# Optimization experiments

Measured on AMD Instinct MI355X. Metric: run time of the kernel, lower is better.

The kernel has to match this reference:

```python
import jax, jax.numpy as jnp
import numpy as np

B, LQ, LK, DK, DV = 32, 128, 4096, 256, 256


def setup_inputs() -> dict:
    key = jax.random.key(0)
    k1, k2, k3, k4, k5 = jax.random.split(key, 5)
    return {
        "query": jax.random.normal(k1, (B, LQ, DK), dtype=jnp.float32),
        "query_lengths": jax.random.randint(k2, (B,), 1, LQ, dtype=jnp.int32),
        "keys": jax.random.normal(k3, (B, LK, DK), dtype=jnp.float32),
        "values": jax.random.normal(k4, (B, LK, DV), dtype=jnp.float32),
        "mask": jax.random.randint(k5, (B, LK), 0, 2, dtype=jnp.int32),  # 1 = masked out
    }


def reference(query, query_lengths, keys, values, mask):
    # zero query positions beyond each example's length (torch: mask_query masked_fill 0)
    q_valid = jnp.arange(query.shape[1])[None, :] < query_lengths[:, None]  # [B, Lq]
    query = jnp.where(q_valid[:, :, None], query, 0.0)
    # zero masked key/value timesteps (torch mask: 1 -> masked)
    kv_valid = (mask == 0)[:, :, None]  # [B, Lk, 1]
    keys = jnp.where(kv_valid, keys, 0.0)
    values = jnp.where(kv_valid, values, 0.0)
    # attention scores [B, Lq, Lk]
    weights = jnp.einsum("bqd,bkd->bqk", query, keys)
    # exact-zero scores (masked rows/cols) -> -inf, matching torch weights==0.0 fill
    weights = jnp.where(weights == 0.0, -jnp.inf, weights)
    weights = jax.nn.softmax(weights, axis=-1)
    # rows that were all -inf produce NaN -> cleaned to 0
    weights = jnp.where(jnp.isnan(weights), 0.0, weights)
    attended = jnp.einsum("bqk,bkv->bqv", weights, values)  # [B, Lq, Dv]
    return jnp.mean(attended, axis=1)  # [B, Dv]
```

## Files before the change

kernel.cpp:

```cpp
#include <hip/hip_runtime.h>
#include <hip/hip_fp16.h>
#include <stdint.h>

#define NB  32
#define NLQ 128
#define NLK 4096
#define NDK 256
#define NDV 256
#define KT  32
#define SPLITS 8
#define MINSPLITS 4

typedef _Float16 f16;
typedef _Float16 f16x4 __attribute__((ext_vector_type(4)));
typedef _Float16 f16x8 __attribute__((ext_vector_type(8)));
typedef float    f32x4 __attribute__((ext_vector_type(4)));

__global__ __launch_bounds__(512) void fvta_part1(
    const float* __restrict__ q_, const float* __restrict__ k_,
    const float* __restrict__ v_, const int* __restrict__ mask_,
    f16* __restrict__ accw, float* __restrict__ mlw)
{
    __shared__ __align__(16) f16 KA[2][KT * NDK];
    __shared__ __align__(16) f16 QA[64 * NDK];
    __shared__ int MK[NLK / MINSPLITS];

    const int tid = threadIdx.x, w = tid >> 6, lane = tid & 63;
    const int l15 = lane & 15, lhi = lane >> 4;
    const int qsub = w >> 1;
    const int dvh  = w & 1;
    const int x = blockIdx.x, b = blockIdx.y;
    const int S = gridDim.x >> 1;
    const int s = x >> 1, qz = x & 1;
    const int slice = NLK / S, nt = slice / KT, kbase = s * slice;
    const float NEG = -__builtin_inff();

    const float* kb = k_ + ((size_t)b * NLK + kbase) * NDK;
    const float* vb = v_ + ((size_t)b * NLK + kbase) * NDV;
    const int*   mb = mask_ + b * NLK + kbase;

    for (int i = tid; i < slice; i += 512) MK[i] = mb[i];

    {
        const float* qsrc = q_ + ((size_t)b * NLQ + qz * 64) * NDK;
        #pragma unroll
        for (int r = 0; r < 8; ++r) {
            const int idx = r * 512 + tid;
            const int qq  = idx >> 6;
            const int d   = (idx & 63) * 4;
            f32x4 xv = *(const f32x4*)(qsrc + qq * NDK + d);
            f16x4 hh; hh[0]=(f16)xv[0]; hh[1]=(f16)xv[1]; hh[2]=(f16)xv[2]; hh[3]=(f16)xv[3];
            *(f16x4*)(QA + qq * NDK + (d ^ ((qq & 15) << 3))) = hh;
        }
    }

    f32x4 accu[8];
    #pragma unroll
    for (int i = 0; i < 8; ++i) accu[i] = (f32x4){0.f, 0.f, 0.f, 0.f};
    float m_run = NEG, l_run = 0.f;

    f32x4 ks[4];

    auto stage = [&](f16* KAb) {
        #pragma unroll
        for (int r = 0; r < 4; ++r) {
            const int idx = r * 512 + tid;
            const int kk  = idx >> 6;
            const int d   = (idx & 63) * 4;
            const int e   = kk * NDK + (d ^ ((kk & 15) << 3));
            f32x4 xv = ks[r];
            f16x4 hh; hh[0]=(f16)xv[0]; hh[1]=(f16)xv[1]; hh[2]=(f16)xv[2]; hh[3]=(f16)xv[3];
            *(f16x4*)(KAb + e) = hh;
        }
    };

    #pragma unroll
    for (int r = 0; r < 4; ++r)
        ks[r] = *(const f32x4*)(kb + (r * 512 + tid) * 4);
    stage(KA[0]);
    __syncthreads();

    const int swz = l15 << 3;

    for (int t = 0; t < nt; ++t) {
        const int cur = t & 1;
        if (t + 1 < nt) {
            const float* ksrc = kb + (size_t)(t + 1) * KT * NDK;
            #pragma unroll
            for (int r = 0; r < 4; ++r)
                ks[r] = *(const f32x4*)(ksrc + (r * 512 + tid) * 4);
        }
        const int k0 = t * KT;

        f32x4 s4a = (f32x4){0.f,0.f,0.f,0.f}, s4b = s4a;
        {
            const f16* k0p = &KA[cur][(0 * 16 + l15) * NDK];
            const f16* k1p = &KA[cur][(1 * 16 + l15) * NDK];
            const f16* qp  = &QA[(qsub * 16 + l15) * NDK];
            #pragma unroll
            for (int kd = 0; kd < 8; ++kd) {
                const int col = (kd * 32 + lhi * 8) ^ swz;
                f16x8 qv  = *(const f16x8*)(qp + col);
                f16x8 kfa = *(const f16x8*)(k0p + col);
                s4a = __builtin_amdgcn_mfma_f32_16x16x32_f16(kfa, qv, s4a, 0, 0, 0);
                f16x8 kfb = *(const f16x8*)(k1p + col);
                s4b = __builtin_amdgcn_mfma_f32_16x16x32_f16(kfb, qv, s4b, 0, 0, 0);
            }
        }

        const int4 m4a = *(const int4*)(MK + k0 + lhi * 4);
        const int4 m4b = *(const int4*)(MK + k0 + 16 + lhi * 4);
        float sa[4], sb[4];
        sa[0] = m4a.x ? NEG : s4a[0]; sa[1] = m4a.y ? NEG : s4a[1];
        sa[2] = m4a.z ? NEG : s4a[2]; sa[3] = m4a.w ? NEG : s4a[3];
        sb[0] = m4b.x ? NEG : s4b[0]; sb[1] = m4b.y ? NEG : s4b[1];
        sb[2] = m4b.z ? NEG : s4b[2]; sb[3] = m4b.w ? NEG : s4b[3];

        float tmax = fmaxf(fmaxf(fmaxf(sa[0], sa[1]), fmaxf(sa[2], sa[3])),
                           fmaxf(fmaxf(sb[0], sb[1]), fmaxf(sb[2], sb[3])));
        tmax = fmaxf(tmax, __shfl_xor(tmax, 16, 64));
        tmax = fmaxf(tmax, __shfl_xor(tmax, 32, 64));

        const bool defer = (m_run != NEG) && __all(tmax - m_run <= 8.f);
        if (!defer) {
            const float mnew = fmaxf(m_run, tmax);
            if (mnew != NEG) {
                const float scale = (m_run == NEG) ? 0.f : __expf(m_run - mnew);
                float scj[4];
                #pragma unroll
                for (int j = 0; j < 4; ++j) scj[j] = __shfl(scale, lhi * 4 + j, 64);
                #pragma unroll
                for (int d = 0; d < 8; ++d) {
                    accu[d][0] *= scj[0]; accu[d][1] *= scj[1];
                    accu[d][2] *= scj[2]; accu[d][3] *= scj[3];
                }
                l_run *= scale;
                m_run = mnew;
            }
        }

        float p4a[4], p4b[4];
        if (m_run == NEG) {
            #pragma unroll
            for (int j = 0; j < 4; ++j) { p4a[j] = 0.f; p4b[j] = 0.f; }
        } else {
            #pragma unroll
            for (int j = 0; j < 4; ++j) {
                p4a[j] = __expf(sa[j] - m_run);
                p4b[j] = __expf(sb[j] - m_run);
            }
        }
        float ps = (p4a[0] + p4a[1]) + (p4a[2] + p4a[3])
                 + (p4b[0] + p4b[1]) + (p4b[2] + p4b[3]);
        ps += __shfl_xor(ps, 16, 64);
        ps += __shfl_xor(ps, 32, 64);
        l_run += ps;

        f16x4 pa, pb;
        pa[0]=(f16)p4a[0]; pa[1]=(f16)p4a[1]; pa[2]=(f16)p4a[2]; pa[3]=(f16)p4a[3];
        pb[0]=(f16)p4b[0]; pb[1]=(f16)p4b[1]; pb[2]=(f16)p4b[2]; pb[3]=(f16)p4b[3];

        {
            #pragma unroll
            for (int h = 0; h < 2; ++h) {
                const f16x4 pfrag = h ? pb : pa;
                const float* vr = vb + (size_t)(k0 + h * 16 + lhi * 4) * NDV
                                + dvh * 128 + l15;
                #pragma unroll
                for (int dg = 0; dg < 2; ++dg) {
                    float tv[4][4];
                    #pragma unroll
                    for (int dd = 0; dd < 4; ++dd) {
                        const float* vc = vr + (dg * 4 + dd) * 16;
                        tv[dd][0] = vc[0];
                        tv[dd][1] = vc[1 * NDV];
                        tv[dd][2] = vc[2 * NDV];
                        tv[dd][3] = vc[3 * NDV];
                    }
                    #pragma unroll
                    for (int dd = 0; dd < 4; ++dd) {
                        f16x4 vf;
                        vf[0]=(f16)tv[dd][0]; vf[1]=(f16)tv[dd][1];
                        vf[2]=(f16)tv[dd][2]; vf[3]=(f16)tv[dd][3];
                        accu[dg * 4 + dd] = __builtin_amdgcn_mfma_f32_16x16x16f16(
                            pfrag, vf, accu[dg * 4 + dd], 0, 0, 0);
                    }
                }
            }
        }

        if (t + 1 < nt) stage(KA[cur ^ 1]);
        __syncthreads();
    }

    const float rl = (l_run > 0.f) ? 1.f / l_run : 0.f;
    float rlj[4];
    #pragma unroll
    for (int j = 0; j < 4; ++j) rlj[j] = __shfl(rl, lhi * 4 + j, 64);

    const size_t base = (size_t)(b * S + s) * NLQ + qz * 64 + qsub * 16;
    #pragma unroll
    for (int j = 0; j < 4; ++j) {
        f16* dst = accw + (base + lhi * 4 + j) * NDV + dvh * 128 + l15;
        #pragma unroll
        for (int d = 0; d < 8; ++d) dst[d * 16] = (f16)(accu[d][j] * rlj[j]);
    }
    if (dvh == 0 && lane < 16) {
        mlw[(base + lane) * 2]     = m_run;
        mlw[(base + lane) * 2 + 1] = l_run;
    }
}

__global__ __launch_bounds__(256) void fvta_merge(
    const f16* __restrict__ accw, const float* __restrict__ mlw,
    const int* __restrict__ qlen_, float* __restrict__ out_, int S)
{
    __shared__ float fac[8][SPLITS + 1];
    const int qc = blockIdx.x, b = blockIdx.y, tid = threadIdx.x;
    const int len = qlen_[b];
    const float NEG = -__builtin_inff();

    if (tid < 8) {
        const int q = qc * 8 + tid;
        if (q < len) {
            float gm = NEG;
            for (int ss = 0; ss < S; ++ss)
                gm = fmaxf(gm, mlw[((size_t)(b * S + ss) * NLQ + q) * 2]);
            float L = 0.f;
            for (int ss = 0; ss < S; ++ss) {
                const float m = mlw[((size_t)(b * S + ss) * NLQ + q) * 2];
                const float l = mlw[((size_t)(b * S + ss) * NLQ + q) * 2 + 1];
                if (m != NEG) L += l * __expf(m - gm);
            }
            for (int ss = 0; ss < S; ++ss) {
                const float m = mlw[((size_t)(b * S + ss) * NLQ + q) * 2];
                const float l = mlw[((size_t)(b * S + ss) * NLQ + q) * 2 + 1];
                fac[tid][ss] = (gm != NEG && L > 0.f && m != NEG)
                             ? l * __expf(m - gm) / L : 0.f;
            }
        } else {
            for (int ss = 0; ss < S; ++ss) fac[tid][ss] = 0.f;
        }
    }
    __syncthreads();

    float sum = 0.f;
    for (int qq = 0; qq < 8; ++qq) {
        const int q = qc * 8 + qq;
        for (int ss = 0; ss < S; ++ss) {
            const float f = fac[qq][ss];
            if (f != 0.f)
                sum += (float)accw[((size_t)(b * S + ss) * NLQ + q) * NDV + tid] * f;
        }
    }
    atomicAdd(&out_[b * NDV + tid], sum * (1.f / NLQ));
}

extern "C" void kernel_launch(void* const* d_in, const int* in_sizes, int n_in,
                              void* d_out, int out_size, void* d_ws, size_t ws_size,
                              hipStream_t stream) {
    const float* q    = (const float*)d_in[0];
    const int*   qlen = (const int*)d_in[1];
    const float* k    = (const float*)d_in[2];
    const float* v    = (const float*)d_in[3];
    const int*   mask = (const int*)d_in[4];
    float* out = (float*)d_out;

    int S = SPLITS;
    while (S > MINSPLITS &&
           ((size_t)NB * S * NLQ * NDV * 2 + (size_t)NB * S * NLQ * 8) > ws_size)
        S >>= 1;
    f16*   accw = (f16*)d_ws;
    float* mlw  = (float*)((char*)d_ws + (size_t)NB * S * NLQ * NDV * 2);

    hipMemsetAsync(out, 0, (size_t)out_size * sizeof(float), stream);
    dim3 g1(2 * S, NB);
    fvta_part1<<<g1, 512, 0, stream>>>(q, k, v, mask, accw, mlw);
    dim3 g2(NLQ / 8, NB);
    fvta_merge<<<g2, 256, 0, stream>>>(accw, mlw, qlen, out, S);
}
```

Measured before the change: 127.4 us.

## Stage V tiles through double-buffered LDS and keep Q fragments in registers

V is now loaded with coalesced vector reads, converted to f16 and double-buffered in LDS alongside K, replacing the strided per-element global loads done inside the PV loop. To free LDS for the new V buffers, the Q tile is no longer staged in shared memory; each wave keeps its Q MFMA fragments in registers for the whole loop. This costs extra registers (qf plus the vs prefetch) and adds scalar f16 LDS reads for V fragments, which may hit bank conflicts and lower occupancy.

```diff
diff --git a/kernel.cpp b/kernel.cpp
--- a/kernel.cpp
+++ b/kernel.cpp
@@ -22,7 +22,7 @@
     f16* __restrict__ accw, float* __restrict__ mlw)
 {
     __shared__ __align__(16) f16 KA[2][KT * NDK];
-    __shared__ __align__(16) f16 QA[64 * NDK];
+    __shared__ __align__(16) f16 VA[2][KT * NDV];
     __shared__ int MK[NLK / MINSPLITS];
 
     const int tid = threadIdx.x, w = tid >> 6, lane = tid & 63;
@@ -41,16 +41,18 @@
 
     for (int i = tid; i < slice; i += 512) MK[i] = mb[i];
 
+    f16x8 qf[8];
     {
-        const float* qsrc = q_ + ((size_t)b * NLQ + qz * 64) * NDK;
+        const float* qrow = q_ + ((size_t)b * NLQ + qz * 64 + qsub * 16 + l15) * NDK
+                          + lhi * 8;
         #pragma unroll
-        for (int r = 0; r < 8; ++r) {
-            const int idx = r * 512 + tid;
-            const int qq  = idx >> 6;
-            const int d   = (idx & 63) * 4;
-            f32x4 xv = *(const f32x4*)(qsrc + qq * NDK + d);
-            f16x4 hh; hh[0]=(f16)xv[0]; hh[1]=(f16)xv[1]; hh[2]=(f16)xv[2]; hh[3]=(f16)xv[3];
-            *(f16x4*)(QA + qq * NDK + (d ^ ((qq & 15) << 3))) = hh;
+        for (int kd = 0; kd < 8; ++kd) {
+            f32x4 xv = *(const f32x4*)(qrow + kd * 32);
+            f32x4 yv = *(const f32x4*)(qrow + kd * 32 + 4);
+            f16x8 f;
+            f[0]=(f16)xv[0]; f[1]=(f16)xv[1]; f[2]=(f16)xv[2]; f[3]=(f16)xv[3];
+            f[4]=(f16)yv[0]; f[5]=(f16)yv[1]; f[6]=(f16)yv[2]; f[7]=(f16)yv[3];
+            qf[kd] = f;
         }
     }
 
@@ -59,9 +61,9 @@
     for (int i = 0; i < 8; ++i) accu[i] = (f32x4){0.f, 0.f, 0.f, 0.f};
     float m_run = NEG, l_run = 0.f;
 
-    f32x4 ks[4];
-
-    auto stage = [&](f16* KAb) {
+    f32x4 ks[4], vs[4];
+
+    auto stage = [&](f16* KAb, f16* VAb) {
         #pragma unroll
         for (int r = 0; r < 4; ++r) {
             const int idx = r * 512 + tid;
@@ -71,13 +73,18 @@
             f32x4 xv = ks[r];
             f16x4 hh; hh[0]=(f16)xv[0]; hh[1]=(f16)xv[1]; hh[2]=(f16)xv[2]; hh[3]=(f16)xv[3];
             *(f16x4*)(KAb + e) = hh;
+            f32x4 yv = vs[r];
+            f16x4 gg; gg[0]=(f16)yv[0]; gg[1]=(f16)yv[1]; gg[2]=(f16)yv[2]; gg[3]=(f16)yv[3];
+            *(f16x4*)(VAb + e) = gg;
         }
     };
 
     #pragma unroll
-    for (int r = 0; r < 4; ++r)
+    for (int r = 0; r < 4; ++r) {
         ks[r] = *(const f32x4*)(kb + (r * 512 + tid) * 4);
-    stage(KA[0]);
+        vs[r] = *(const f32x4*)(vb + (r * 512 + tid) * 4);
+    }
+    stage(KA[0], VA[0]);
     __syncthreads();
 
     const int swz = l15 << 3;
@@ -86,9 +93,12 @@
         const int cur = t & 1;
         if (t + 1 < nt) {
             const float* ksrc = kb + (size_t)(t + 1) * KT * NDK;
-            #pragma unroll
-            for (int r = 0; r < 4; ++r)
+            const float* vsrc = vb + (size_t)(t + 1) * KT * NDV;
+            #pragma unroll
+            for (int r = 0; r < 4; ++r) {
                 ks[r] = *(const f32x4*)(ksrc + (r * 512 + tid) * 4);
+                vs[r] = *(const f32x4*)(vsrc + (r * 512 + tid) * 4);
+            }
         }
         const int k0 = t * KT;
 
@@ -96,15 +106,13 @@
         {
             const f16* k0p = &KA[cur][(0 * 16 + l15) * NDK];
             const f16* k1p = &KA[cur][(1 * 16 + l15) * NDK];
-            const f16* qp  = &QA[(qsub * 16 + l15) * NDK];
             #pragma unroll
             for (int kd = 0; kd < 8; ++kd) {
                 const int col = (kd * 32 + lhi * 8) ^ swz;
-                f16x8 qv  = *(const f16x8*)(qp + col);
                 f16x8 kfa = *(const f16x8*)(k0p + col);
-                s4a = __builtin_amdgcn_mfma_f32_16x16x32_f16(kfa, qv, s4a, 0, 0, 0);
+                s4a = __builtin_amdgcn_mfma_f32_16x16x32_f16(kfa, qf[kd], s4a, 0, 0, 0);
                 f16x8 kfb = *(const f16x8*)(k1p + col);
-                s4b = __builtin_amdgcn_mfma_f32_16x16x32_f16(kfb, qv, s4b, 0, 0, 0);
+                s4b = __builtin_amdgcn_mfma_f32_16x16x32_f16(kfb, qf[kd], s4b, 0, 0, 0);
             }
         }
 
@@ -161,27 +169,23 @@
         pb[0]=(f16)p4b[0]; pb[1]=(f16)p4b[1]; pb[2]=(f16)p4b[2]; pb[3]=(f16)p4b[3];
 
         {
+            const f16* VL = &VA[cur][0];
             #pragma unroll
             for (int h = 0; h < 2; ++h) {
                 const f16x4 pfrag = h ? pb : pa;
-                const float* vr = vb + (size_t)(k0 + h * 16 + lhi * 4) * NDV
-                                + dvh * 128 + l15;
                 #pragma unroll
                 for (int dg = 0; dg < 2; ++dg) {
-                    float tv[4][4];
-                    #pragma unroll
-                    for (int dd = 0; dd < 4; ++dd) {
-                        const float* vc = vr + (dg * 4 + dd) * 16;
-                        tv[dd][0] = vc[0];
-                        tv[dd][1] = vc[1 * NDV];
-                        tv[dd][2] = vc[2 * NDV];
-                        tv[dd][3] = vc[3 * NDV];
-                    }
                     #pragma unroll
                     for (int dd = 0; dd < 4; ++dd) {
                         f16x4 vf;
-                        vf[0]=(f16)tv[dd][0]; vf[1]=(f16)tv[dd][1];
-                        vf[2]=(f16)tv[dd][2]; vf[3]=(f16)tv[dd][3];
+                        #pragma unroll
+                        for (int j = 0; j < 4; ++j) {
+                            const int rr  = lhi * 4 + j;
+                            const int row = h * 16 + rr;
+                            const int col = (dvh * 128 + (dg * 4 + dd) * 16 + l15)
+                                            ^ (rr << 3);
+                            vf[j] = VL[row * NDV + col];
+                        }
                         accu[dg * 4 + dd] = __builtin_amdgcn_mfma_f32_16x16x16f16(
                             pfrag, vf, accu[dg * 4 + dd], 0, 0, 0);
                     }
@@ -189,7 +193,7 @@
             }
         }
 
-        if (t + 1 < nt) stage(KA[cur ^ 1]);
+        if (t + 1 < nt) stage(KA[cur ^ 1], VA[cur ^ 1]);
         __syncthreads();
     }
 
```

Result: no change. 127.8 us (+0.3%).
